# Performance work log

Measured on AMD Instinct MI355X. Metric: run time of the kernel, lower is better.

The kernel has to match this reference:

```python
import jax, jax.numpy as jnp
import numpy as np

VOCAB, EMB, T = 10000, 100, 80
UNITS, BATCH = 256, 4096


def setup_inputs() -> dict:
    key = jax.random.key(0)
    ks = jax.random.split(key, 8)
    s = lambda k, shape, scale: jax.random.normal(k, shape, jnp.float32) * scale
    return {
        "inputs": jax.random.randint(ks[0], (BATCH, T), 0, VOCAB, dtype=jnp.int32),
        "emb": s(ks[1], (VOCAB, EMB), 0.05),
        "W1": s(ks[2], (EMB, UNITS), 1.0 / np.sqrt(EMB)),
        "U1": s(ks[3], (UNITS, UNITS), 1.0 / np.sqrt(UNITS)),
        "b1": jnp.zeros((UNITS,), jnp.float32),
        "W2": s(ks[4], (UNITS, UNITS), 1.0 / np.sqrt(UNITS)),
        "U2": s(ks[5], (UNITS, UNITS), 1.0 / np.sqrt(UNITS)),
        "b2": jnp.zeros((UNITS,), jnp.float32),
        "Wd": s(ks[6], (UNITS, 1), 1.0 / np.sqrt(UNITS)),
        "bd": jnp.zeros((1,), jnp.float32),
    }


def _simple_rnn(xs, W, U, b, return_sequences):
    # xs: [B, T, D]; h_t = tanh(x_t @ W + h_{t-1} @ U + b) (Keras SimpleRNN, eval mode)
    B = xs.shape[0]
    H = U.shape[0]
    xproj = jnp.einsum('btd,dh->bth', xs, W) + b  # precompute input projection
    h0 = jnp.zeros((B, H), xs.dtype)

    def step(h, xp):
        h = jnp.tanh(xp + h @ U)
        return h, h

    hT, hs = jax.lax.scan(step, h0, jnp.swapaxes(xproj, 0, 1))  # scan over time
    return jnp.swapaxes(hs, 0, 1) if return_sequences else hT


def reference(inputs, emb, W1, U1, b1, W2, U2, b2, Wd, bd):
    x = emb[inputs]                                   # [B, T, EMB]
    x = _simple_rnn(x, W1, U1, b1, return_sequences=True)   # [B, T, UNITS]
    x = _simple_rnn(x, W2, U2, b2, return_sequences=False)  # [B, UNITS]
    s = x @ Wd + bd  # computed in original but unused in returned value
    del s
    return jax.nn.sigmoid(x)                          # original returns sigmoid(x), not sigmoid(s)
```

## Files before the change

### kernel.cpp

```cpp
#include <hip/hip_runtime.h>

#define BATCH 4096
#define TLEN  80
#define EMBD  100
#define UNITS 256

typedef _Float16 f16;
typedef __attribute__((ext_vector_type(8))) _Float16 h8;
typedef __attribute__((ext_vector_type(4))) _Float16 h4;
typedef __attribute__((ext_vector_type(4))) float f32x4;

__device__ __forceinline__ float fast_tanh(float x) {
  float ax = __builtin_fabsf(x);
  float e  = __expf(-2.f * ax);
  float r  = (1.f - e) * __builtin_amdgcn_rcpf(1.f + e);
  return __builtin_copysignf(r, x);
}
__device__ __forceinline__ float fast_sigmoid(float x) {
  return __builtin_amdgcn_rcpf(1.f + __expf(-x));
}

__device__ __forceinline__ void block_sync_lds() {
  asm volatile("s_waitcnt lgkmcnt(0)\n\ts_barrier" ::: "memory");
}

#define KT_ALL 28
#define OFF_P1 ((size_t)0)
#define P1_BYTES ((size_t)10000 * UNITS * 2)
#define OFF_WF  P1_BYTES
#define WF_BYTES ((size_t)KT_ALL * 16 * 64 * 8 * 2)
#define WS_NEED (OFF_WF + WF_BYTES)

__device__ __forceinline__ size_t fidx(int ktg, int nt, int lane) {
  return (((size_t)ktg * 16 + nt) * 64 + lane) * 8;
}

__global__ __launch_bounds__(256) void k_split_w16(
    const float* __restrict__ W1, const float* __restrict__ U1,
    const float* __restrict__ W2, const float* __restrict__ U2,
    f16* __restrict__ wf)
{
  int gid = blockIdx.x * 256 + threadIdx.x;
  if (gid >= KT_ALL * 16 * 64) return;
  int lane = gid & 63, nt = (gid >> 6) & 15, ktg = gid >> 10;
  const float* M; int Kact, ktl;
  if (ktg < 4)       { M = W1; Kact = EMBD;  ktl = ktg;      }
  else if (ktg < 12) { M = U1; Kact = UNITS; ktl = ktg - 4;  }
  else if (ktg < 20) { M = W2; Kact = UNITS; ktl = ktg - 12; }
  else               { M = U2; Kact = UNITS; ktl = ktg - 20; }
  int n = nt * 16 + (lane & 15);
  int kb = ktl * 32 + (lane >> 4) * 8;
  size_t base = fidx(ktg, nt, lane);
#pragma unroll
  for (int j = 0; j < 8; ++j) {
    int k = kb + j;
    wf[base + j] = (f16)((k < Kact) ? M[(size_t)k * UNITS + n] : 0.f);
  }
}

__global__ __launch_bounds__(256) void k_p1(
    const float* __restrict__ emb, const float* __restrict__ W1,
    const float* __restrict__ b1, f16* __restrict__ p1t)
{
  __shared__ float er[16][EMBD];
  const int v0 = blockIdx.x * 16;
  for (int i = threadIdx.x; i < 16 * EMBD; i += 256) {
    int vv = i / EMBD, kk = i - vv * EMBD;
    er[vv][kk] = emb[(size_t)(v0 + vv) * EMBD + kk];
  }
  __syncthreads();
  const int n = threadIdx.x;
  float acc[16];
  const float bb = b1[n];
#pragma unroll
  for (int vv = 0; vv < 16; ++vv) acc[vv] = bb;
  for (int k = 0; k < EMBD; ++k) {
    float w = W1[(size_t)k * UNITS + n];
#pragma unroll
    for (int vv = 0; vv < 16; ++vv) acc[vv] += er[vv][k] * w;
  }
#pragma unroll
  for (int vv = 0; vv < 16; ++vv)
    p1t[(size_t)(v0 + vv) * UNITS + n] = (f16)acc[vv];
}

#define MFMA16(A, B, C) __builtin_amdgcn_mfma_f32_16x16x32_f16(A, B, C, 0, 0, 0)

__device__ __forceinline__ void store_row4(f16* __restrict__ f, int nb, int m,
                                           float v0, float v1, float v2, float v3) {
  int a = (nb >> 5) * 512 + (((nb >> 3) & 3) * 16 + m) * 8 + (nb & 7);
  h4 p; p[0] = (f16)v0; p[1] = (f16)v1; p[2] = (f16)v2; p[3] = (f16)v3;
  *(h4*)&f[a] = p;
}

__global__ __launch_bounds__(512, 2)
__attribute__((amdgpu_waves_per_eu(2, 2)))
void rnn_wsG(
    const int* __restrict__ idx, const f16* __restrict__ p1t,
    const f16* __restrict__ wf, const float* __restrict__ b2,
    float* __restrict__ out)
{
  __shared__ __align__(16) f16 f1[2][4096];
  __shared__ __align__(16) f16 f2[2][4096];
  extern __shared__ f16 u2s[];

  const int tid  = threadIdx.x;
  const int lane = tid & 63;
  const int w    = tid >> 6;
  const int m    = lane & 15;
  const int q    = lane >> 4;
  const int b0   = blockIdx.x * 16;
  const int n0b  = 32 * w + 4 * q;
  const int n1b  = n0b + 16;

  const f32x4 b2v0 = *(const f32x4*)&b2[n0b];
  const f32x4 b2v1 = *(const f32x4*)&b2[n1b];

  const int* tokm = idx + (size_t)(b0 + m) * TLEN;
  const f16* __restrict__ p1g = p1t + n0b;

  for (int d = tid; d < 4096; d += 512) {
    int l = d & 63, g = d >> 6, no = g >> 3, kt = g & 7;
    *(h8*)&u2s[(size_t)d * 8] = *(const h8*)(wf + fidx(20 + kt, 2 * no + 1, l));
  }

  h8 Bu1a[8], Bu1b[8], Bw2a[8], Bw2b[8], Bu2a[8];
#pragma unroll
  for (int kt = 0; kt < 8; ++kt) {
    Bu1a[kt] = *(const h8*)(wf + fidx(4 + kt, 2 * w, lane));
    Bu1b[kt] = *(const h8*)(wf + fidx(4 + kt, 2 * w + 1, lane));
    Bw2a[kt] = *(const h8*)(wf + fidx(12 + kt, 2 * w, lane));
    Bw2b[kt] = *(const h8*)(wf + fidx(12 + kt, 2 * w + 1, lane));
    Bu2a[kt] = *(const h8*)(wf + fidx(20 + kt, 2 * w, lane));
  }
#pragma unroll
  for (int kt = 0; kt < 8; ++kt) {
    asm volatile("" : "+v"(Bu1a[kt])); asm volatile("" : "+v"(Bu1b[kt]));
    asm volatile("" : "+v"(Bw2a[kt])); asm volatile("" : "+v"(Bw2b[kt]));
    asm volatile("" : "+v"(Bu2a[kt]));
  }

  for (int i = tid; i < 4096; i += 512) f2[0][i] = (f16)0.f;

  {
    const f16* pr = p1g + (size_t)tokm[0] * UNITS;
    h4 v0 = *(const h4*)(pr);
    h4 v1 = *(const h4*)(pr + 16);
    store_row4(f1[0], n0b, m, fast_tanh((float)v0[0]), fast_tanh((float)v0[1]),
                              fast_tanh((float)v0[2]), fast_tanh((float)v0[3]));
    store_row4(f1[0], n1b, m, fast_tanh((float)v1[0]), fast_tanh((float)v1[1]),
                              fast_tanh((float)v1[2]), fast_tanh((float)v1[3]));
  }

  h4 pv0, pv1;
  {
    const f16* pr = p1g + (size_t)tokm[1] * UNITS;
    pv0 = *(const h4*)(pr);
    pv1 = *(const h4*)(pr + 16);
  }
  int tkn = tokm[2];
  __syncthreads();

#define RNN_STEP(RD, WR, STAGE, TKI)                                         \
  {                                                                          \
    f32x4 x0, x1;                                                            \
    _Pragma("unroll")                                                        \
    for (int r = 0; r < 4; ++r) {                                            \
      x0[r] = (float)pv0[r];                                                 \
      x1[r] = (float)pv1[r];                                                 \
    }                                                                        \
    if (STAGE) {                                                             \
      const f16* pr_ = p1g + (size_t)tkn * UNITS;                            \
      pv0 = *(const h4*)(pr_);                                               \
      pv1 = *(const h4*)(pr_ + 16);                                          \
    }                                                                        \
    tkn = tokm[TKI];                                                         \
    f32x4 yA0 = b2v0, yA1 = b2v1;                                            \
    f32x4 yB0 = (f32x4){0.f, 0.f, 0.f, 0.f};                                 \
    f32x4 yB1 = (f32x4){0.f, 0.f, 0.f, 0.f};                                 \
    _Pragma("unroll")                                                        \
    for (int kt = 0; kt < 8; ++kt) {                                         \
      h8 a1 = *(const h8*)&f1[RD][kt * 512 + lane * 8];                      \
      h8 a2 = *(const h8*)&f2[RD][kt * 512 + lane * 8];                      \
      h8 ub = *(const h8*)&u2s[((w * 8 + kt) * 64 + lane) * 8];              \
      x0  = MFMA16(Bu1a[kt], a1, x0);                                        \
      x1  = MFMA16(Bu1b[kt], a1, x1);                                        \
      yA0 = MFMA16(Bw2a[kt], a1, yA0);                                       \
      yA1 = MFMA16(Bw2b[kt], a1, yA1);                                       \
      yB0 = MFMA16(Bu2a[kt], a2, yB0);                                       \
      yB1 = MFMA16(ub,       a2, yB1);                                       \
    }                                                                        \
    store_row4(f1[WR], n0b, m, fast_tanh(x0[0]), fast_tanh(x0[1]),           \
                               fast_tanh(x0[2]), fast_tanh(x0[3]));          \
    store_row4(f1[WR], n1b, m, fast_tanh(x1[0]), fast_tanh(x1[1]),           \
                               fast_tanh(x1[2]), fast_tanh(x1[3]));          \
    store_row4(f2[WR], n0b, m,                                               \
               fast_tanh(yA0[0] + yB0[0]), fast_tanh(yA0[1] + yB0[1]),       \
               fast_tanh(yA0[2] + yB0[2]), fast_tanh(yA0[3] + yB0[3]));      \
    store_row4(f2[WR], n1b, m,                                               \
               fast_tanh(yA1[0] + yB1[0]), fast_tanh(yA1[1] + yB1[1]),       \
               fast_tanh(yA1[2] + yB1[2]), fast_tanh(yA1[3] + yB1[3]));      \
    block_sync_lds();                                                        \
  }

  for (int i = 1; i < TLEN - 1; i += 2) {
    int t2 = i + 3 < TLEN - 1 ? i + 3 : TLEN - 1;
    RNN_STEP(0, 1, true, i + 2);
    RNN_STEP(1, 0, true, t2);
  }
  RNN_STEP(0, 1, false, TLEN - 1);
#undef RNN_STEP

  {
    f32x4 yA0 = b2v0, yA1 = b2v1;
    f32x4 yB0 = (f32x4){0.f, 0.f, 0.f, 0.f};
    f32x4 yB1 = (f32x4){0.f, 0.f, 0.f, 0.f};
#pragma unroll
    for (int kt = 0; kt < 8; ++kt) {
      h8 a1 = *(const h8*)&f1[1][kt * 512 + lane * 8];
      h8 a2 = *(const h8*)&f2[1][kt * 512 + lane * 8];
      h8 ub = *(const h8*)&u2s[((w * 8 + kt) * 64 + lane) * 8];
      yA0 = MFMA16(Bw2a[kt], a1, yA0);
      yA1 = MFMA16(Bw2b[kt], a1, yA1);
      yB0 = MFMA16(Bu2a[kt], a2, yB0);
      yB1 = MFMA16(ub,       a2, yB1);
    }
    f32x4 o0, o1;
#pragma unroll
    for (int r = 0; r < 4; ++r) {
      o0[r] = fast_sigmoid(fast_tanh(yA0[r] + yB0[r]));
      o1[r] = fast_sigmoid(fast_tanh(yA1[r] + yB1[r]));
    }
    *(f32x4*)&out[(size_t)(b0 + m) * UNITS + n0b] = o0;
    *(f32x4*)&out[(size_t)(b0 + m) * UNITS + n1b] = o1;
  }
}

extern "C" void kernel_launch(void* const* d_in, const int* in_sizes, int n_in,
                              void* d_out, int out_size, void* d_ws, size_t ws_size,
                              hipStream_t stream)
{
  const int*   idx = (const int*)d_in[0];
  const float* emb = (const float*)d_in[1];
  const float* W1  = (const float*)d_in[2];
  const float* U1  = (const float*)d_in[3];
  const float* b1  = (const float*)d_in[4];
  const float* W2  = (const float*)d_in[5];
  const float* U2  = (const float*)d_in[6];
  const float* b2  = (const float*)d_in[7];
  float* out = (float*)d_out;

  static bool attr_done = false;
  if (!attr_done) {
    (void)hipFuncSetAttribute((const void*)rnn_wsG,
                              hipFuncAttributeMaxDynamicSharedMemorySize,
                              65536);
    attr_done = true;
  }

  f16* p1t = (f16*)((char*)d_ws + OFF_P1);
  f16* wf  = (f16*)((char*)d_ws + OFF_WF);
  k_p1<<<10000 / 16, 256, 0, stream>>>(emb, W1, b1, p1t);
  k_split_w16<<<(KT_ALL * 16 * 64 + 255) / 256, 256, 0, stream>>>(W1, U1, W2, U2, wf);
  rnn_wsG<<<BATCH / 16, 512, 65536, stream>>>(idx, p1t, wf, b2, out);
}
```

Measured before the change: 218.7 us.

## Specialize waves: half run layer-1 recurrence, half run layer-2 recurrence

The block's eight waves are split into two groups. Four waves compute the layer-1 recurrence over all 256 units, and four compute the layer-2 input and recurrent products. The full U2 matrix moves into LDS, which doubles dynamic shared memory to 128KB. Each wave now keeps a single 4x8 set of B fragments in registers instead of five sets of eight. The split is uneven: layer-2 waves issue twice as many MFMAs per step as layer-1 waves, plus extra LDS reads, so the per-step barrier may wait on the heavier group.

```diff
diff --git a/kernel.cpp b/kernel.cpp
--- a/kernel.cpp
+++ b/kernel.cpp
@@ -95,7 +95,7 @@
 
 __global__ __launch_bounds__(512, 2)
 __attribute__((amdgpu_waves_per_eu(2, 2)))
-void rnn_wsG(
+void rnn_wsH(
     const int* __restrict__ idx, const f16* __restrict__ p1t,
     const f16* __restrict__ wf, const float* __restrict__ b2,
     float* __restrict__ out)
@@ -107,99 +107,112 @@
   const int tid  = threadIdx.x;
   const int lane = tid & 63;
   const int w    = tid >> 6;
+  const bool g0  = (w < 4);
+  const int wt   = g0 ? w : w - 4;
   const int m    = lane & 15;
   const int q    = lane >> 4;
   const int b0   = blockIdx.x * 16;
-  const int n0b  = 32 * w + 4 * q;
-  const int n1b  = n0b + 16;
-
-  const f32x4 b2v0 = *(const f32x4*)&b2[n0b];
-  const f32x4 b2v1 = *(const f32x4*)&b2[n1b];
-
+
+  int nb[4];
+#pragma unroll
+  for (int j = 0; j < 4; ++j) nb[j] = 64 * wt + 16 * j + 4 * q;
+
+  for (int d = tid; d < 8192; d += 512) {
+    int l = d & 63, g = d >> 6, t = g >> 3, kt = g & 7;
+    *(h8*)&u2s[(size_t)d * 8] = *(const h8*)(wf + fidx(20 + kt, t, l));
+  }
+
+  h8 Bp[4][8];
+  {
+    const int ktg0 = g0 ? 4 : 12;
+#pragma unroll
+    for (int j = 0; j < 4; ++j)
+#pragma unroll
+      for (int kt = 0; kt < 8; ++kt)
+        Bp[j][kt] = *(const h8*)(wf + fidx(ktg0 + kt, 4 * wt + j, lane));
+  }
+#pragma unroll
+  for (int j = 0; j < 4; ++j)
+#pragma unroll
+    for (int kt = 0; kt < 8; ++kt)
+      asm volatile("" : "+v"(Bp[j][kt]));
+
+  f32x4 b2v[4];
+  if (!g0) {
+#pragma unroll
+    for (int j = 0; j < 4; ++j) b2v[j] = *(const f32x4*)&b2[nb[j]];
+  }
   const int* tokm = idx + (size_t)(b0 + m) * TLEN;
-  const f16* __restrict__ p1g = p1t + n0b;
-
-  for (int d = tid; d < 4096; d += 512) {
-    int l = d & 63, g = d >> 6, no = g >> 3, kt = g & 7;
-    *(h8*)&u2s[(size_t)d * 8] = *(const h8*)(wf + fidx(20 + kt, 2 * no + 1, l));
-  }
-
-  h8 Bu1a[8], Bu1b[8], Bw2a[8], Bw2b[8], Bu2a[8];
-#pragma unroll
-  for (int kt = 0; kt < 8; ++kt) {
-    Bu1a[kt] = *(const h8*)(wf + fidx(4 + kt, 2 * w, lane));
-    Bu1b[kt] = *(const h8*)(wf + fidx(4 + kt, 2 * w + 1, lane));
-    Bw2a[kt] = *(const h8*)(wf + fidx(12 + kt, 2 * w, lane));
-    Bw2b[kt] = *(const h8*)(wf + fidx(12 + kt, 2 * w + 1, lane));
-    Bu2a[kt] = *(const h8*)(wf + fidx(20 + kt, 2 * w, lane));
-  }
-#pragma unroll
-  for (int kt = 0; kt < 8; ++kt) {
-    asm volatile("" : "+v"(Bu1a[kt])); asm volatile("" : "+v"(Bu1b[kt]));
-    asm volatile("" : "+v"(Bw2a[kt])); asm volatile("" : "+v"(Bw2b[kt]));
-    asm volatile("" : "+v"(Bu2a[kt]));
-  }
 
   for (int i = tid; i < 4096; i += 512) f2[0][i] = (f16)0.f;
 
-  {
-    const f16* pr = p1g + (size_t)tokm[0] * UNITS;
-    h4 v0 = *(const h4*)(pr);
-    h4 v1 = *(const h4*)(pr + 16);
-    store_row4(f1[0], n0b, m, fast_tanh((float)v0[0]), fast_tanh((float)v0[1]),
-                              fast_tanh((float)v0[2]), fast_tanh((float)v0[3]));
-    store_row4(f1[0], n1b, m, fast_tanh((float)v1[0]), fast_tanh((float)v1[1]),
-                              fast_tanh((float)v1[2]), fast_tanh((float)v1[3]));
-  }
-
-  h4 pv0, pv1;
-  {
-    const f16* pr = p1g + (size_t)tokm[1] * UNITS;
-    pv0 = *(const h4*)(pr);
-    pv1 = *(const h4*)(pr + 16);
-  }
-  int tkn = tokm[2];
+  h4 pv[4];
+  int tkn = 0;
+  if (g0) {
+    const f16* pr = p1t + (size_t)tokm[0] * UNITS;
+#pragma unroll
+    for (int j = 0; j < 4; ++j) {
+      h4 v = *(const h4*)(pr + nb[j]);
+      store_row4(f1[0], nb[j], m, fast_tanh((float)v[0]), fast_tanh((float)v[1]),
+                                  fast_tanh((float)v[2]), fast_tanh((float)v[3]));
+    }
+    const f16* pr1 = p1t + (size_t)tokm[1] * UNITS;
+#pragma unroll
+    for (int j = 0; j < 4; ++j) pv[j] = *(const h4*)(pr1 + nb[j]);
+    tkn = tokm[2];
+  }
   __syncthreads();
 
 #define RNN_STEP(RD, WR, STAGE, TKI)                                         \
   {                                                                          \
-    f32x4 x0, x1;                                                            \
-    _Pragma("unroll")                                                        \
-    for (int r = 0; r < 4; ++r) {                                            \
-      x0[r] = (float)pv0[r];                                                 \
-      x1[r] = (float)pv1[r];                                                 \
+    if (g0) {                                                                \
+      f32x4 x[4];                                                            \
+      _Pragma("unroll")                                                      \
+      for (int j = 0; j < 4; ++j)                                            \
+        _Pragma("unroll")                                                    \
+        for (int r = 0; r < 4; ++r) x[j][r] = (float)pv[j][r];               \
+      if (STAGE) {                                                           \
+        const f16* pr_ = p1t + (size_t)tkn * UNITS;                          \
+        _Pragma("unroll")                                                    \
+        for (int j = 0; j < 4; ++j) pv[j] = *(const h4*)(pr_ + nb[j]);       \
+      }                                                                      \
+      tkn = tokm[TKI];                                                       \
+      _Pragma("unroll")                                                      \
+      for (int kt = 0; kt < 8; ++kt) {                                       \
+        h8 a1 = *(const h8*)&f1[RD][kt * 512 + lane * 8];                    \
+        _Pragma("unroll")                                                    \
+        for (int j = 0; j < 4; ++j) x[j] = MFMA16(Bp[j][kt], a1, x[j]);      \
+      }                                                                      \
+      _Pragma("unroll")                                                      \
+      for (int j = 0; j < 4; ++j)                                            \
+        store_row4(f1[WR], nb[j], m, fast_tanh(x[j][0]), fast_tanh(x[j][1]), \
+                                     fast_tanh(x[j][2]), fast_tanh(x[j][3]));\
+    } else {                                                                 \
+      f32x4 yA[4], yB[4];                                                    \
+      _Pragma("unroll")                                                      \
+      for (int j = 0; j < 4; ++j) {                                          \
+        yA[j] = b2v[j];                                                      \
+        yB[j] = (f32x4){0.f, 0.f, 0.f, 0.f};                                 \
+      }                                                                      \
+      _Pragma("unroll")                                                      \
+      for (int kt = 0; kt < 8; ++kt) {                                       \
+        h8 a1 = *(const h8*)&f1[RD][kt * 512 + lane * 8];                    \
+        h8 a2 = *(const h8*)&f2[RD][kt * 512 + lane * 8];                    \
+        _Pragma("unroll")                                                    \
+        for (int j = 0; j < 4; ++j) {                                        \
+          h8 ub = *(const h8*)&u2s[(((4 * wt + j) * 8 + kt) * 64 + lane) * 8];\
+          yA[j] = MFMA16(Bp[j][kt], a1, yA[j]);                              \
+          yB[j] = MFMA16(ub,        a2, yB[j]);                              \
+        }                                                                    \
+      }                                                                      \
+      _Pragma("unroll")                                                      \
+      for (int j = 0; j < 4; ++j)                                            \
+        store_row4(f2[WR], nb[j], m,                                         \
+                   fast_tanh(yA[j][0] + yB[j][0]),                           \
+                   fast_tanh(yA[j][1] + yB[j][1]),                           \
+                   fast_tanh(yA[j][2] + yB[j][2]),                           \
+                   fast_tanh(yA[j][3] + yB[j][3]));                          \
     }                                                                        \
-    if (STAGE) {                                                             \
-      const f16* pr_ = p1g + (size_t)tkn * UNITS;                            \
-      pv0 = *(const h4*)(pr_);                                               \
-      pv1 = *(const h4*)(pr_ + 16);                                          \
-    }                                                                        \
-    tkn = tokm[TKI];                                                         \
-    f32x4 yA0 = b2v0, yA1 = b2v1;                                            \
-    f32x4 yB0 = (f32x4){0.f, 0.f, 0.f, 0.f};                                 \
-    f32x4 yB1 = (f32x4){0.f, 0.f, 0.f, 0.f};                                 \
-    _Pragma("unroll")                                                        \
-    for (int kt = 0; kt < 8; ++kt) {                                         \
-      h8 a1 = *(const h8*)&f1[RD][kt * 512 + lane * 8];                      \
-      h8 a2 = *(const h8*)&f2[RD][kt * 512 + lane * 8];                      \
-      h8 ub = *(const h8*)&u2s[((w * 8 + kt) * 64 + lane) * 8];              \
-      x0  = MFMA16(Bu1a[kt], a1, x0);                                        \
-      x1  = MFMA16(Bu1b[kt], a1, x1);                                        \
-      yA0 = MFMA16(Bw2a[kt], a1, yA0);                                       \
-      yA1 = MFMA16(Bw2b[kt], a1, yA1);                                       \
-      yB0 = MFMA16(Bu2a[kt], a2, yB0);                                       \
-      yB1 = MFMA16(ub,       a2, yB1);                                       \
-    }                                                                        \
-    store_row4(f1[WR], n0b, m, fast_tanh(x0[0]), fast_tanh(x0[1]),           \
-                               fast_tanh(x0[2]), fast_tanh(x0[3]));          \
-    store_row4(f1[WR], n1b, m, fast_tanh(x1[0]), fast_tanh(x1[1]),           \
-                               fast_tanh(x1[2]), fast_tanh(x1[3]));          \
-    store_row4(f2[WR], n0b, m,                                               \
-               fast_tanh(yA0[0] + yB0[0]), fast_tanh(yA0[1] + yB0[1]),       \
-               fast_tanh(yA0[2] + yB0[2]), fast_tanh(yA0[3] + yB0[3]));      \
-    store_row4(f2[WR], n1b, m,                                               \
-               fast_tanh(yA1[0] + yB1[0]), fast_tanh(yA1[1] + yB1[1]),       \
-               fast_tanh(yA1[2] + yB1[2]), fast_tanh(yA1[3] + yB1[3]));      \
     block_sync_lds();                                                        \
   }
 
@@ -211,28 +224,32 @@
   RNN_STEP(0, 1, false, TLEN - 1);
 #undef RNN_STEP
 
-  {
-    f32x4 yA0 = b2v0, yA1 = b2v1;
-    f32x4 yB0 = (f32x4){0.f, 0.f, 0.f, 0.f};
-    f32x4 yB1 = (f32x4){0.f, 0.f, 0.f, 0.f};
+  if (!g0) {
+    f32x4 yA[4], yB[4];
+#pragma unroll
+    for (int j = 0; j < 4; ++j) {
+      yA[j] = b2v[j];
+      yB[j] = (f32x4){0.f, 0.f, 0.f, 0.f};
+    }
 #pragma unroll
     for (int kt = 0; kt < 8; ++kt) {
       h8 a1 = *(const h8*)&f1[1][kt * 512 + lane * 8];
       h8 a2 = *(const h8*)&f2[1][kt * 512 + lane * 8];
-      h8 ub = *(const h8*)&u2s[((w * 8 + kt) * 64 + lane) * 8];
-      yA0 = MFMA16(Bw2a[kt], a1, yA0);
-      yA1 = MFMA16(Bw2b[kt], a1, yA1);
-      yB0 = MFMA16(Bu2a[kt], a2, yB0);
-      yB1 = MFMA16(ub,       a2, yB1);
-    }
-    f32x4 o0, o1;
-#pragma unroll
-    for (int r = 0; r < 4; ++r) {
-      o0[r] = fast_sigmoid(fast_tanh(yA0[r] + yB0[r]));
-      o1[r] = fast_sigmoid(fast_tanh(yA1[r] + yB1[r]));
-    }
-    *(f32x4*)&out[(size_t)(b0 + m) * UNITS + n0b] = o0;
-    *(f32x4*)&out[(size_t)(b0 + m) * UNITS + n1b] = o1;
+#pragma unroll
+      for (int j = 0; j < 4; ++j) {
+        h8 ub = *(const h8*)&u2s[(((4 * wt + j) * 8 + kt) * 64 + lane) * 8];
+        yA[j] = MFMA16(Bp[j][kt], a1, yA[j]);
+        yB[j] = MFMA16(ub,        a2, yB[j]);
+      }
+    }
+#pragma unroll
+    for (int j = 0; j < 4; ++j) {
+      f32x4 o;
+#pragma unroll
+      for (int r = 0; r < 4; ++r)
+        o[r] = fast_sigmoid(fast_tanh(yA[j][r] + yB[j][r]));
+      *(f32x4*)&out[(size_t)(b0 + m) * UNITS + nb[j]] = o;
+    }
   }
 }
 
@@ -252,9 +269,9 @@
 
   static bool attr_done = false;
   if (!attr_done) {
-    (void)hipFuncSetAttribute((const void*)rnn_wsG,
+    (void)hipFuncSetAttribute((const void*)rnn_wsH,
                               hipFuncAttributeMaxDynamicSharedMemorySize,
-                              65536);
+                              131072);
     attr_done = true;
   }
 
@@ -262,5 +279,5 @@
   f16* wf  = (f16*)((char*)d_ws + OFF_WF);
   k_p1<<<10000 / 16, 256, 0, stream>>>(emb, W1, b1, p1t);
   k_split_w16<<<(KT_ALL * 16 * 64 + 255) / 256, 256, 0, stream>>>(W1, U1, W2, U2, wf);
-  rnn_wsG<<<BATCH / 16, 512, 65536, stream>>>(idx, p1t, wf, b2, out);
-}
+  rnn_wsH<<<BATCH / 16, 512, 131072, stream>>>(idx, p1t, wf, b2, out);
+}
```

After: 227.7 us. 1.04x slower.
